# Kernel tuning notes

Measured on AMD Instinct MI355X. Metric: run time of the kernel, lower is better.

## Reference

```python
import jax, jax.numpy as jnp
import numpy as np

BN_EPS = 1e-5
TEMPERATURE = 256 ** 0.5  # sqrt(c2), since cv3 = ScaledDotProductAttention(c2)


def conv_bn_silu(x, w, gamma, beta, mean, var):
    # Conv2d(k=3, s=1, pad='same', bias=False) -> BatchNorm2d (running stats) -> SiLU
    y = jax.lax.conv_general_dilated(
        x, w, window_strides=(1, 1), padding='SAME',
        dimension_numbers=('NCHW', 'OIHW', 'NCHW'))
    scale = (gamma / jnp.sqrt(var + BN_EPS))[None, :, None, None]
    shift = (beta - mean * gamma / jnp.sqrt(var + BN_EPS))[None, :, None, None]
    y = y * scale + shift
    return y * jax.nn.sigmoid(y)  # SiLU


def setup_inputs() -> dict:
    key = jax.random.key(0)
    ks = jax.random.split(key, 8)
    B, C, H, W = 16, 256, 64, 64
    Ch = 128  # hidden channels c_ = int(c2 * e)
    x = jax.random.normal(ks[0], (B, C, H, W), dtype=jnp.float32)
    w1 = jax.random.normal(ks[1], (Ch, C, 3, 3), dtype=jnp.float32) * 0.05
    g1 = jnp.ones((Ch,), jnp.float32) + 0.1 * jax.random.normal(ks[2], (Ch,), dtype=jnp.float32)
    b1 = 0.1 * jax.random.normal(ks[3], (Ch,), dtype=jnp.float32)
    m1 = 0.1 * jax.random.normal(ks[4], (Ch,), dtype=jnp.float32)
    v1 = jnp.ones((Ch,), jnp.float32) + 0.5 * jax.random.uniform(ks[5], (Ch,), dtype=jnp.float32)
    w2 = jax.random.normal(ks[6], (C, Ch, 3, 3), dtype=jnp.float32) * 0.05
    g2 = jnp.ones((C,), jnp.float32)
    b2 = jnp.zeros((C,), jnp.float32)
    m2 = 0.1 * jax.random.normal(ks[7], (C,), dtype=jnp.float32)
    v2 = jnp.ones((C,), jnp.float32) + 0.5 * jax.random.uniform(jax.random.fold_in(key, 99), (C,), dtype=jnp.float32)
    return {"x": x, "w1": w1, "g1": g1, "b1": b1, "m1": m1, "v1": v1,
            "w2": w2, "g2": g2, "b2": b2, "m2": m2, "v2": v2}


def reference(x, w1, g1, b1, m1, v1, w2, g2, b2, m2, v2):
    y = conv_bn_silu(x, w1, g1, b1, m1, v1)       # [B, 128, H, W]
    y = conv_bn_silu(y, w2, g2, b2, m2, v2)       # [B, 256, H, W]
    B, C, H, W = y.shape
    q = y.reshape(B, C, H * W)                    # q = k^T = v, all views of y
    # channel-channel attention: scores [B, C, C]
    scores = jnp.einsum('bcn,bdn->bcd', q / TEMPERATURE, q)
    attn = jax.nn.softmax(scores, axis=-1)        # dropout is identity in eval
    out = jnp.einsum('bcd,bdn->bcn', attn, q).reshape(B, C, H, W)
    return x + out  # shortcut: c1 == c2
```

## Files before the change

kernel.cpp:

```cpp
#include <hip/hip_runtime.h>
#include <math.h>

#define BB 16
#define C1 256
#define CHD 128
#define NN 4096
#define INV_T (1.0f/16.0f)

typedef _Float16 half8 __attribute__((ext_vector_type(8)));
typedef __attribute__((ext_vector_type(4))) float f32x4;
typedef __attribute__((ext_vector_type(16))) float f32x16;

__device__ inline unsigned short f2h(float f) {
    _Float16 h = (_Float16)f;
    return __builtin_bit_cast(unsigned short, h);
}

#define GLDS(g, l) __builtin_amdgcn_global_load_lds(                              \
    (const __attribute__((address_space(1))) unsigned int*)(g),                   \
    (__attribute__((address_space(3))) unsigned int*)(l), 16, 0, 0)

__device__ inline void xcd_remap(int& bx, int& by, int& bz) {
    int gx = gridDim.x, gy = gridDim.y;
    int lin = blockIdx.x + gx * (blockIdx.y + gy * blockIdx.z);
    int cpx = (gx * gy * (int)gridDim.z) >> 3;
    lin = (lin & 7) * cpx + (lin >> 3);
    bx = lin % gx; int t = lin / gx; by = t % gy; bz = t / gy;
}

__global__ __launch_bounds__(256) void nchw_to_nhwc_f16(
    const float* __restrict__ x, unsigned short* __restrict__ xh, int C)
{
    const int c0 = blockIdx.x * 64;
    const int hp = blockIdx.y;
    const int b  = blockIdx.z;
    const int nCk = C >> 4;

    if (hp == 0 || hp == 65) {
        for (int idx = threadIdx.x; idx < 1024; idx += 256) {
            int w = idx >> 4, cq = (idx & 15) * 4;
            int ck = (c0 >> 4) + (cq >> 4), half = (cq >> 3) & 1, rem = cq & 7;
            ushort4 z; z.x = z.y = z.z = z.w = 0;
            *(ushort4*)&xh[(((((size_t)b * nCk + ck) * 66 + hp) * 2 + half) * 64 + w) * 8
                           + rem] = z;
        }
        return;
    }
    const int h = hp - 1;
    __shared__ float ts[64][65];
    for (int idx = threadIdx.x; idx < 4096; idx += 256) {
        int cl = idx >> 6, w = idx & 63;
        ts[cl][w] = x[(((size_t)b * C + c0 + cl) * 64 + h) * 64 + w];
    }
    __syncthreads();
    for (int idx = threadIdx.x; idx < 1024; idx += 256) {
        int w = idx >> 4, cq = (idx & 15) * 4;
        int ck = (c0 >> 4) + (cq >> 4), half = (cq >> 3) & 1, rem = cq & 7;
        ushort4 o;
        o.x = f2h(ts[cq + 0][w]); o.y = f2h(ts[cq + 1][w]);
        o.z = f2h(ts[cq + 2][w]); o.w = f2h(ts[cq + 3][w]);
        *(ushort4*)&xh[(((((size_t)b * nCk + ck) * 66 + hp) * 2 + half) * 64 + w) * 8
                       + rem] = o;
    }
}

__global__ __launch_bounds__(256) void pack_w_kernel(
    const float* __restrict__ w, unsigned short* __restrict__ wT, int Cout, int Cin)
{
    int idx = blockIdx.x * 256 + threadIdx.x;
    int total = Cout * Cin * 9;
    if (idx >= total) return;
    int ci = idx % Cin; int t = idx / Cin; int co = t % Cout; int kk = t / Cout;
    int ck = ci >> 4, half = (ci >> 3) & 1, rem = ci & 7;
    wT[((((size_t)ck * 9 + kk) * 2 + half) * Cout + co) * 8 + rem] =
        f2h(w[((size_t)co * Cin + ci) * 9 + kk]);
}

__global__ __launch_bounds__(256) void zero_y1h_pads(unsigned short* __restrict__ y1h)
{
    int idx = blockIdx.x * 256 + threadIdx.x;
    int b   = idx >> 12;
    int ck  = (idx >> 9) & 7;
    int row = ((idx >> 8) & 1) ? 65 : 0;
    int inner = (idx & 255) * 4;
    ushort4 z; z.x = z.y = z.z = z.w = 0;
    *(ushort4*)&y1h[(((size_t)b * 8 + ck) * 66 + row) * 1024 + inner] = z;
}

__global__ __launch_bounds__(512, 4) void conv_mfma_kernel(
    const unsigned short* __restrict__ xh, const unsigned short* __restrict__ wT,
    const float* __restrict__ gamma, const float* __restrict__ beta,
    const float* __restrict__ mean, const float* __restrict__ var,
    unsigned short* __restrict__ outNHWC,
    unsigned short* __restrict__ yhi, unsigned short* __restrict__ yhiT,
    int Cin, int Cout)
{
    int bx, by, bz;
    xcd_remap(bx, by, bz);
    const int tid  = threadIdx.x;
    const int wid  = tid >> 6;
    const int lane = tid & 63;
    const int l31  = lane & 31;
    const int hi   = lane >> 5;
    const int coBase = bx * 64;
    const int h0     = by * 8;
    const int b      = bz;
    const int nCk    = Cin >> 4;

    __shared__ __align__(16) unsigned short smem[39552];
    __shared__ float bnsc[64], bnsh[64];

    if (tid < 64) {
        int co = coBase + tid;
        float sc = gamma[co] * rsqrtf(var[co] + 1e-5f);
        bnsc[tid] = sc;
        bnsh[tid] = beta[co] - mean[co] * sc;
    }
    if (tid < 80) {
        int buf  = tid & 1;
        int col  = ((tid >> 1) & 1) ? 65 : 0;
        int half = (tid >> 2) & 1;
        int r    = tid >> 3;
        ushort4 z; z.x = z.y = z.z = z.w = 0;
        *(ushort4*)&smem[buf * 10560 + ((r * 2 + half) * 66 + col) * 8] = z;
        *(ushort4*)&smem[buf * 10560 + ((r * 2 + half) * 66 + col) * 8 + 4] = z;
    }

    auto stage = [&](int sel, int ck) {
        unsigned short* wsd = smem + 21120 + sel * 9216;
        unsigned short* xsd = smem + sel * 10560;
        for (int it = wid; it < 38; it += 8) {
            if (it < 18) {
                int kk = it >> 1, half = it & 1;
                const unsigned short* g =
                    wT + ((((size_t)ck * 9 + kk) * 2 + half) * Cout + coBase) * 8 + lane * 8;
                GLDS(g, wsd + (kk * 2 + half) * 512);
            } else {
                int j = it - 18;
                int r = j >> 1, half = j & 1;
                const unsigned short* g =
                    xh + ((((size_t)b * nCk + ck) * 66 + h0 + r) * 2 + half) * 512 + lane * 8;
                GLDS(g, xsd + ((r * 2 + half) * 66 + 1) * 8);
            }
        }
    };

    stage(0, 0);
    __syncthreads();

    f32x16 acc[2][2] = {};

    int sel = 0;
    for (int ck = 0; ck < nCk; ck++) {
        if (ck + 1 < nCk) stage(sel ^ 1, ck + 1);

        const unsigned short* wsb = smem + 21120 + sel * 9216;
        const unsigned short* xsb = smem + sel * 10560;
        __builtin_amdgcn_s_setprio(1);
#pragma unroll
        for (int kk = 0; kk < 9; kk++) {
            const int kh = kk / 3, kw = kk % 3;
            half8 a0 = *(const half8*)&wsb[((kk * 2 + hi) * 64 +      l31) * 8];
            half8 a1 = *(const half8*)&wsb[((kk * 2 + hi) * 64 + 32 + l31) * 8];
            const unsigned short* xr =
                &xsb[(((wid + kh) * 2 + hi) * 66 + l31 + kw) * 8];
            half8 b0 = *(const half8*)xr;
            half8 b1 = *(const half8*)&xr[32 * 8];
            acc[0][0] = __builtin_amdgcn_mfma_f32_32x32x16_f16(a0, b0, acc[0][0], 0, 0, 0);
            acc[0][1] = __builtin_amdgcn_mfma_f32_32x32x16_f16(a0, b1, acc[0][1], 0, 0, 0);
            acc[1][0] = __builtin_amdgcn_mfma_f32_32x32x16_f16(a1, b0, acc[1][0], 0, 0, 0);
            acc[1][1] = __builtin_amdgcn_mfma_f32_32x32x16_f16(a1, b1, acc[1][1], 0, 0, 0);
        }
        __builtin_amdgcn_s_setprio(0);
        __syncthreads();
        sel ^= 1;
    }

    const int orow = h0 + wid;
    const bool isConv1 = (outNHWC != nullptr);

    __syncthreads();

#pragma unroll
    for (int mi = 0; mi < 2; mi++)
#pragma unroll
        for (int ni = 0; ni < 2; ni++) {
            f32x16 a = acc[mi][ni];
            int w = ni * 32 + l31;
            int swz = ((l31 + wid) & 7) << 3;
#pragma unroll
            for (int rq = 0; rq < 4; rq++) {
                int c0 = mi * 32 + rq * 8 + hi * 4;
                ushort4 o; unsigned short* op = (unsigned short*)&o;
#pragma unroll
                for (int r = 0; r < 4; r++) {
                    float t = a[rq * 4 + r] * bnsc[c0 + r] + bnsh[c0 + r];
                    float s = t / (1.f + __expf(-t));
                    op[r] = f2h(s);
                    if (!isConv1)
                        yhi[(((size_t)b * Cout + coBase + c0 + r) * 64 + orow) * 64 + w] = op[r];
                }
                *(ushort4*)&smem[wid * 4096 + w * 64 + (c0 ^ swz)] = o;
            }
        }
    __syncthreads();

    const int ckB = bx * 4;
    const int nCkOut = Cout >> 4;
#pragma unroll
    for (int j = 0; j < 8; j++) {
        int g   = j * 512 + tid;
        int s   = g & 1;
        int w   = (g >> 1) & 63;
        int row = (g >> 7) & 7;
        int ck  = g >> 10;
        uint4 v = *(const uint4*)&smem[row * 4096 + w * 64 +
                     (((ck * 2 + s) * 8) ^ (((w + row) & 7) << 3))];
        if (isConv1) {
            *(uint4*)&outNHWC[((((((size_t)b * nCkOut + ckB + ck) * 66 + h0 + row + 1) * 2 + s)
                               * 64 + w) * 8)] = v;
        } else {
            *(uint4*)&yhiT[(((size_t)b * nCkOut + ckB + ck) * 4096 + (size_t)(h0 + row) * 64 + w) * 16
                           + s * 8] = v;
        }
    }
}

__global__ __launch_bounds__(256) void scores_mfma_kernel(
    const unsigned short* __restrict__ yhi, float* __restrict__ scores)
{
    static const int TI[10] = {0,0,0,0,1,1,1,2,2,3};
    static const int TJ[10] = {0,1,2,3,1,2,3,2,3,3};
    int bx, by, bz;
    xcd_remap(bx, by, bz);
    const int b  = bz;
    const int kh = by;
    const int ti = TI[bx], tj = TJ[bx];
    const int cB = ti * 64;
    const int dB = tj * 64;
    const int tid  = threadIdx.x;
    const int wid  = tid >> 6;
    const int lane = tid & 63;
    const int ln   = lane & 15;
    const int q    = lane >> 4;
    const int wm   = wid >> 1, wn = wid & 1;

    float* scp = scores + (size_t)kh * 1048576;

    __shared__ unsigned short As[64 * 128];
    __shared__ unsigned short Bs[64 * 128];

    const int rl = lane >> 4;
    const int gl = lane & 15;

    f32x4 acc[2][2] = {};

    for (int ck = kh * 16; ck < kh * 16 + 16; ck++) {
        const int n0 = ck * 128;
        for (int it = wid; it < 32; it += 4) {
            const int tile = it >> 4;
            const int j = it & 15;
            const int r = j * 4 + rl;
            const int gq = gl ^ (r & 7);
            const int rowAbs = (tile ? dB : cB) + r;
            const unsigned short* g =
                yhi + ((size_t)b * 256 + rowAbs) * 4096 + n0 + gq * 8;
            GLDS(g, (tile ? Bs : As) + j * 512);
        }
        __syncthreads();

#pragma unroll
        for (int kwin = 0; kwin < 4; kwin++) {
            half8 ah[2], bh[2];
#pragma unroll
            for (int mi = 0; mi < 2; mi++) {
                int row = wm * 32 + mi * 16 + ln;
                ah[mi] = *(const half8*)&As[row * 128 + ((kwin * 4 + q) ^ (ln & 7)) * 8];
            }
#pragma unroll
            for (int ni = 0; ni < 2; ni++) {
                int row = wn * 32 + ni * 16 + ln;
                bh[ni] = *(const half8*)&Bs[row * 128 + ((kwin * 4 + q) ^ (ln & 7)) * 8];
            }
#pragma unroll
            for (int mi = 0; mi < 2; mi++)
#pragma unroll
                for (int ni = 0; ni < 2; ni++)
                    acc[mi][ni] = __builtin_amdgcn_mfma_f32_16x16x32_f16(
                        ah[mi], bh[ni], acc[mi][ni], 0, 0, 0);
        }
        __syncthreads();
    }

#pragma unroll
    for (int mi = 0; mi < 2; mi++)
#pragma unroll
        for (int ni = 0; ni < 2; ni++) {
            f32x4 a = acc[mi][ni];
            float vals[4];
            vals[0] = a.x * INV_T; vals[1] = a.y * INV_T;
            vals[2] = a.z * INV_T; vals[3] = a.w * INV_T;
            int c0 = cB + wm * 32 + mi * 16 + q * 4;
            int d  = dB + wn * 32 + ni * 16 + ln;
#pragma unroll
            for (int r = 0; r < 4; r++)
                scp[((size_t)b * C1 + c0 + r) * C1 + d] = vals[r];
            if (ti != tj) {
                float4 tv = {vals[0], vals[1], vals[2], vals[3]};
                *(float4*)&scp[((size_t)b * C1 + d) * C1 + c0] = tv;
            }
        }
}

__global__ __launch_bounds__(64) void softmax_kernel(
    const float* __restrict__ scores, unsigned short* __restrict__ attn16)
{
    const int row = blockIdx.x;
    const float* p = scores + (size_t)row * C1;
    const int lane = threadIdx.x;

    float4 v0 = ((const float4*)p)[lane];
    float4 v1 = ((const float4*)(p + 1048576))[lane];
    float4 v;
    v.x = v0.x + v1.x; v.y = v0.y + v1.y;
    v.z = v0.z + v1.z; v.w = v0.w + v1.w;
    float m = fmaxf(fmaxf(v.x, v.y), fmaxf(v.z, v.w));
#pragma unroll
    for (int off = 32; off >= 1; off >>= 1)
        m = fmaxf(m, __shfl_xor(m, off, 64));

    float4 e;
    e.x = expf(v.x - m); e.y = expf(v.y - m);
    e.z = expf(v.z - m); e.w = expf(v.w - m);
    float s = e.x + e.y + e.z + e.w;
#pragma unroll
    for (int off = 32; off >= 1; off >>= 1)
        s += __shfl_xor(s, off, 64);
    float inv = 1.f / s;
    ushort4 o;
    o.x = f2h(e.x * inv); o.y = f2h(e.y * inv);
    o.z = f2h(e.z * inv); o.w = f2h(e.w * inv);
    *(ushort4*)&attn16[(size_t)row * C1 + lane * 4] = o;
}

__global__ __launch_bounds__(256) void out_mfma_kernel(
    const unsigned short* __restrict__ attn16, const unsigned short* __restrict__ yhiT,
    const float* __restrict__ x, float* __restrict__ out)
{
    int bx, by, bz;
    xcd_remap(bx, by, bz);
    const int b  = bz;
    const int cB = by * 64;
    const int nB = bx * 128;
    const int tid  = threadIdx.x;
    const int wid  = tid >> 6;
    const int lane = tid & 63;
    const int ln   = lane & 15;
    const int q    = lane >> 4;
    const int wm   = wid >> 1, wn = wid & 1;

    __shared__ unsigned short As[64 * 64];
    __shared__ unsigned short Bs[4 * 128 * 16];

    const int r8 = lane >> 3;
    const int gq = (lane & 7) ^ r8;

    f32x4 acc[2][4] = {};

    for (int ck = 0; ck < 4; ck++) {
        const int d0 = ck * 64;
        for (int it = wid; it < 24; it += 4) {
            if (it < 8) {
                const unsigned short* g =
                    attn16 + ((size_t)b * 256 + cB + it * 8 + r8) * 256 + d0 + gq * 8;
                GLDS(g, As + it * 512);
            } else {
                int j = it - 8;
                int u = j >> 2, part = j & 3;
                const unsigned short* g =
                    yhiT + (((size_t)b * 16 + ck * 4 + u) * 4096 + nB + part * 32) * 16 + lane * 8;
                GLDS(g, Bs + (u * 128 + part * 32) * 16);
            }
        }
        __syncthreads();

#pragma unroll
        for (int kwin = 0; kwin < 2; kwin++) {
            const int cc = (((kwin * 4 + q) ^ (ln & 7))) * 8;
            const int gK = kwin * 4 + q;
            half8 af[2], bfr[4];
#pragma unroll
            for (int mi = 0; mi < 2; mi++)
                af[mi] = *(const half8*)&As[(wm * 32 + mi * 16 + ln) * 64 + cc];
#pragma unroll
            for (int ni = 0; ni < 4; ni++) {
                int row = wn * 64 + ni * 16 + ln;
                bfr[ni] = *(const half8*)&Bs[(gK >> 1) * 2048 + row * 16 + (gK & 1) * 8];
            }
#pragma unroll
            for (int mi = 0; mi < 2; mi++)
#pragma unroll
                for (int ni = 0; ni < 4; ni++)
                    acc[mi][ni] = __builtin_amdgcn_mfma_f32_16x16x32_f16(
                        af[mi], bfr[ni], acc[mi][ni], 0, 0, 0);
        }
        __syncthreads();
    }

#pragma unroll
    for (int mi = 0; mi < 2; mi++)
#pragma unroll
        for (int ni = 0; ni < 4; ni++) {
            f32x4 a = acc[mi][ni];
            float vals[4] = {a.x, a.y, a.z, a.w};
#pragma unroll
            for (int r = 0; r < 4; r++) {
                int c = cB + wm * 32 + mi * 16 + q * 4 + r;
                int n = nB + wn * 64 + ni * 16 + ln;
                size_t o = ((size_t)b * C1 + c) * NN + n;
                out[o] = x[o] + vals[r];
            }
        }
}

extern "C" void kernel_launch(void* const* d_in, const int* in_sizes, int n_in,
                              void* d_out, int out_size, void* d_ws, size_t ws_size,
                              hipStream_t stream)
{
    const float* x  = (const float*)d_in[0];
    const float* w1 = (const float*)d_in[1];
    const float* g1 = (const float*)d_in[2];
    const float* b1 = (const float*)d_in[3];
    const float* m1 = (const float*)d_in[4];
    const float* v1 = (const float*)d_in[5];
    const float* w2 = (const float*)d_in[6];
    const float* g2 = (const float*)d_in[7];
    const float* b2 = (const float*)d_in[8];
    const float* m2 = (const float*)d_in[9];
    const float* v2 = (const float*)d_in[10];
    float* out = (float*)d_out;

    unsigned short* xh   = (unsigned short*)d_ws;
    unsigned short* y1h  = xh  + (size_t)17301504;
    unsigned short* wt1  = y1h + (size_t)8650752;
    unsigned short* wt2  = wt1 + (size_t)294912;
    unsigned short* yhiT = wt2 + (size_t)294912;
    unsigned short* yhi  = xh;
    float*          sc   = (float*)y1h;
    unsigned short* attn16 = (unsigned short*)(sc + 2097152);

    nchw_to_nhwc_f16<<<dim3(C1 / 64, 66, BB), 256, 0, stream>>>(x, xh, C1);
    pack_w_kernel<<<(9 * CHD * C1 + 255) / 256, 256, 0, stream>>>(w1, wt1, CHD, C1);
    pack_w_kernel<<<(9 * C1 * CHD + 255) / 256, 256, 0, stream>>>(w2, wt2, C1, CHD);
    zero_y1h_pads<<<256, 256, 0, stream>>>(y1h);

    conv_mfma_kernel<<<dim3(CHD / 64, 8, BB), 512, 0, stream>>>(
        xh, wt1, g1, b1, m1, v1, y1h, nullptr, nullptr, C1, CHD);
    conv_mfma_kernel<<<dim3(C1 / 64, 8, BB), 512, 0, stream>>>(
        y1h, wt2, g2, b2, m2, v2, nullptr, yhi, yhiT, CHD, C1);

    scores_mfma_kernel<<<dim3(10, 2, BB), 256, 0, stream>>>(yhi, sc);
    softmax_kernel<<<dim3(BB * C1), 64, 0, stream>>>(sc, attn16);
    out_mfma_kernel<<<dim3(NN / 128, 4, BB), 256, 0, stream>>>(attn16, yhiT, x, out);
}
```

Before: 307.5 us.

## Vectorize loads/stores, merge prep kernels, split scores K into three parts

The NCHW-to-NHWC transpose now reads x with float4 loads. The weight packing and pad zeroing are merged into one prep kernel, removing two launches. The scores GEMM splits the K dimension three ways instead of two (11/11/10 chunks) to launch more blocks, and softmax sums three partial buffers. The output kernel stages its accumulators in shared memory so it can do coalesced float4 residual loads and stores. In exchange, the scores stage writes an extra partial buffer and the output epilogue adds an LDS round trip.

```diff
diff --git a/kernel.cpp b/kernel.cpp
--- a/kernel.cpp
+++ b/kernel.cpp
@@ -48,9 +48,11 @@
     }
     const int h = hp - 1;
     __shared__ float ts[64][65];
-    for (int idx = threadIdx.x; idx < 4096; idx += 256) {
-        int cl = idx >> 6, w = idx & 63;
-        ts[cl][w] = x[(((size_t)b * C + c0 + cl) * 64 + h) * 64 + w];
+    for (int idx = threadIdx.x; idx < 1024; idx += 256) {
+        int cl = idx >> 4, w4 = (idx & 15) * 4;
+        float4 v = *(const float4*)&x[(((size_t)b * C + c0 + cl) * 64 + h) * 64 + w4];
+        ts[cl][w4 + 0] = v.x; ts[cl][w4 + 1] = v.y;
+        ts[cl][w4 + 2] = v.z; ts[cl][w4 + 3] = v.w;
     }
     __syncthreads();
     for (int idx = threadIdx.x; idx < 1024; idx += 256) {
@@ -64,27 +66,33 @@
     }
 }
 
-__global__ __launch_bounds__(256) void pack_w_kernel(
-    const float* __restrict__ w, unsigned short* __restrict__ wT, int Cout, int Cin)
-{
+__global__ __launch_bounds__(256) void prep_kernel(
+    const float* __restrict__ w1, const float* __restrict__ w2,
+    unsigned short* __restrict__ wt1, unsigned short* __restrict__ wt2,
+    unsigned short* __restrict__ y1h)
+{
+    const int P = 9 * CHD * C1;
     int idx = blockIdx.x * 256 + threadIdx.x;
-    int total = Cout * Cin * 9;
-    if (idx >= total) return;
-    int ci = idx % Cin; int t = idx / Cin; int co = t % Cout; int kk = t / Cout;
-    int ck = ci >> 4, half = (ci >> 3) & 1, rem = ci & 7;
-    wT[((((size_t)ck * 9 + kk) * 2 + half) * Cout + co) * 8 + rem] =
-        f2h(w[((size_t)co * Cin + ci) * 9 + kk]);
-}
-
-__global__ __launch_bounds__(256) void zero_y1h_pads(unsigned short* __restrict__ y1h)
-{
-    int idx = blockIdx.x * 256 + threadIdx.x;
-    int b   = idx >> 12;
-    int ck  = (idx >> 9) & 7;
-    int row = ((idx >> 8) & 1) ? 65 : 0;
-    int inner = (idx & 255) * 4;
-    ushort4 z; z.x = z.y = z.z = z.w = 0;
-    *(ushort4*)&y1h[(((size_t)b * 8 + ck) * 66 + row) * 1024 + inner] = z;
+    if (idx < P) {
+        int ci = idx % C1; int t = idx / C1; int co = t % CHD; int kk = t / CHD;
+        int ck = ci >> 4, half = (ci >> 3) & 1, rem = ci & 7;
+        wt1[((((size_t)ck * 9 + kk) * 2 + half) * CHD + co) * 8 + rem] =
+            f2h(w1[((size_t)co * C1 + ci) * 9 + kk]);
+    } else if (idx < 2 * P) {
+        idx -= P;
+        int ci = idx % CHD; int t = idx / CHD; int co = t % C1; int kk = t / C1;
+        int ck = ci >> 4, half = (ci >> 3) & 1, rem = ci & 7;
+        wt2[((((size_t)ck * 9 + kk) * 2 + half) * C1 + co) * 8 + rem] =
+            f2h(w2[((size_t)co * CHD + ci) * 9 + kk]);
+    } else {
+        idx -= 2 * P;
+        int b   = idx >> 12;
+        int ck  = (idx >> 9) & 7;
+        int row = ((idx >> 8) & 1) ? 65 : 0;
+        int inner = (idx & 255) * 4;
+        ushort4 z; z.x = z.y = z.z = z.w = 0;
+        *(ushort4*)&y1h[(((size_t)b * 8 + ck) * 66 + row) * 1024 + inner] = z;
+    }
 }
 
 __global__ __launch_bounds__(512, 4) void conv_mfma_kernel(
@@ -255,7 +263,8 @@
 
     f32x4 acc[2][2] = {};
 
-    for (int ck = kh * 16; ck < kh * 16 + 16; ck++) {
+    const int ckEnd = (kh == 2) ? 32 : kh * 11 + 11;
+    for (int ck = kh * 11; ck < ckEnd; ck++) {
         const int n0 = ck * 128;
         for (int it = wid; it < 32; it += 4) {
             const int tile = it >> 4;
@@ -321,9 +330,10 @@
 
     float4 v0 = ((const float4*)p)[lane];
     float4 v1 = ((const float4*)(p + 1048576))[lane];
+    float4 v2 = ((const float4*)(p + 2097152))[lane];
     float4 v;
-    v.x = v0.x + v1.x; v.y = v0.y + v1.y;
-    v.z = v0.z + v1.z; v.w = v0.w + v1.w;
+    v.x = v0.x + v1.x + v2.x; v.y = v0.y + v1.y + v2.y;
+    v.z = v0.z + v1.z + v2.z; v.w = v0.w + v1.w + v2.w;
     float m = fmaxf(fmaxf(v.x, v.y), fmaxf(v.z, v.w));
 #pragma unroll
     for (int off = 32; off >= 1; off >>= 1)
@@ -359,8 +369,9 @@
     const int q    = lane >> 4;
     const int wm   = wid >> 1, wn = wid & 1;
 
-    __shared__ unsigned short As[64 * 64];
-    __shared__ unsigned short Bs[4 * 128 * 16];
+    __shared__ __align__(16) unsigned short smem[16896];
+    unsigned short* As = smem;
+    unsigned short* Bs = smem + 4096;
 
     const int r8 = lane >> 3;
     const int gq = (lane & 7) ^ r8;
@@ -407,20 +418,34 @@
         __syncthreads();
     }
 
+    float* os = (float*)smem;
 #pragma unroll
     for (int mi = 0; mi < 2; mi++)
 #pragma unroll
         for (int ni = 0; ni < 4; ni++) {
             f32x4 a = acc[mi][ni];
-            float vals[4] = {a.x, a.y, a.z, a.w};
-#pragma unroll
-            for (int r = 0; r < 4; r++) {
-                int c = cB + wm * 32 + mi * 16 + q * 4 + r;
-                int n = nB + wn * 64 + ni * 16 + ln;
-                size_t o = ((size_t)b * C1 + c) * NN + n;
-                out[o] = x[o] + vals[r];
-            }
-        }
+            int cl = wm * 32 + mi * 16 + q * 4;
+            int nl = wn * 64 + ni * 16 + ln;
+            os[(cl + 0) * 132 + nl] = a.x;
+            os[(cl + 1) * 132 + nl] = a.y;
+            os[(cl + 2) * 132 + nl] = a.z;
+            os[(cl + 3) * 132 + nl] = a.w;
+        }
+    __syncthreads();
+
+#pragma unroll
+    for (int j = 0; j < 8; j++) {
+        int u  = j * 256 + tid;
+        int c  = u >> 5;
+        int nq = (u & 31) * 4;
+        float4 ov = *(const float4*)&os[c * 132 + nq];
+        size_t go = ((size_t)b * C1 + cB + c) * NN + nB + nq;
+        float4 xv = *(const float4*)&x[go];
+        float4 o4;
+        o4.x = ov.x + xv.x; o4.y = ov.y + xv.y;
+        o4.z = ov.z + xv.z; o4.w = ov.w + xv.w;
+        *(float4*)&out[go] = o4;
+    }
 }
 
 extern "C" void kernel_launch(void* const* d_in, const int* in_sizes, int n_in,
@@ -447,19 +472,17 @@
     unsigned short* yhiT = wt2 + (size_t)294912;
     unsigned short* yhi  = xh;
     float*          sc   = (float*)y1h;
-    unsigned short* attn16 = (unsigned short*)(sc + 2097152);
+    unsigned short* attn16 = (unsigned short*)(sc + 3145728);
 
     nchw_to_nhwc_f16<<<dim3(C1 / 64, 66, BB), 256, 0, stream>>>(x, xh, C1);
-    pack_w_kernel<<<(9 * CHD * C1 + 255) / 256, 256, 0, stream>>>(w1, wt1, CHD, C1);
-    pack_w_kernel<<<(9 * C1 * CHD + 255) / 256, 256, 0, stream>>>(w2, wt2, C1, CHD);
-    zero_y1h_pads<<<256, 256, 0, stream>>>(y1h);
+    prep_kernel<<<2560, 256, 0, stream>>>(w1, w2, wt1, wt2, y1h);
 
     conv_mfma_kernel<<<dim3(CHD / 64, 8, BB), 512, 0, stream>>>(
         xh, wt1, g1, b1, m1, v1, y1h, nullptr, nullptr, C1, CHD);
     conv_mfma_kernel<<<dim3(C1 / 64, 8, BB), 512, 0, stream>>>(
         y1h, wt2, g2, b2, m2, v2, nullptr, yhi, yhiT, CHD, C1);
 
-    scores_mfma_kernel<<<dim3(10, 2, BB), 256, 0, stream>>>(yhi, sc);
+    scores_mfma_kernel<<<dim3(10, 3, BB), 256, 0, stream>>>(yhi, sc);
     softmax_kernel<<<dim3(BB * C1), 64, 0, stream>>>(sc, attn16);
     out_mfma_kernel<<<dim3(NN / 128, 4, BB), 256, 0, stream>>>(attn16, yhiT, x, out);
 }
```

Result: faster. 278.9 us (-9.3%).
